# Kernel optimization log

Hardware: AMD Instinct MI355X
Metric: run time of the kernel (lower is better)

## Reference

```python
import jax, jax.numpy as jnp
import numpy as np

D_DIM = 1024
K_DIM = 16
B, L = 4, 2048

def setup_inputs() -> dict:
    key = jax.random.key(0)
    kx, ky, kz, kw, kb = jax.random.split(key, 5)
    x = jax.random.normal(kx, (B, L, D_DIM), dtype=jnp.float32)
    y = jax.random.normal(ky, (B, L, D_DIM), dtype=jnp.float32)
    z = jax.random.normal(kz, (B, L, D_DIM), dtype=jnp.float32)
    bound = 1.0 / np.sqrt(3 * D_DIM)  # torch Linear init scale
    W = jax.random.uniform(kw, (K_DIM * D_DIM, 3 * D_DIM), dtype=jnp.float32, minval=-bound, maxval=bound)
    b = jax.random.uniform(kb, (K_DIM * D_DIM,), dtype=jnp.float32, minval=-bound, maxval=bound)
    return {"x": x, "y": y, "z": z, "W": W, "b": b}

def reference(x, y, z, W, b):
    Bsz, Lsz, D = x.shape
    inp = jnp.concatenate([x, y, z], axis=-1)                 # (B, L, 3D)
    kernel = jnp.einsum('blc,fc->blf', inp, W) + b            # (B, L, k*D)
    kernel = kernel.reshape(Bsz, Lsz, D, K_DIM)               # (B, L, D, k)
    # einsum 'bldk,bld->bld' == sum over k, then elementwise multiply
    return kernel.sum(axis=-1) * (x * y)
```

## Files before the change

### kernel.cpp

```cpp
#include <hip/hip_runtime.h>

#define M_ROWS 8192
#define N_DIM  1024
#define K3     3072
#define KD     16
#define NKT    48
#define BM     256
#define BN     128
#define BK     64
#define LDS_A  (BM * BK)
#define LDS_B  (BN * BK)
#define LDS_TILE (LDS_A + LDS_B)

typedef __bf16 bf16x8 __attribute__((ext_vector_type(8)));
typedef float  f32x4  __attribute__((ext_vector_type(4)));

__device__ __forceinline__ unsigned short f2bf(float f) {
  return __builtin_bit_cast(unsigned short, (__bf16)f);
}
__device__ __forceinline__ float bf2f(unsigned short u) {
  return __builtin_bit_cast(float, (unsigned int)u << 16);
}
__device__ __forceinline__ ushort4 pack4(float4 f) {
  ushort4 o; o.x = f2bf(f.x); o.y = f2bf(f.y); o.z = f2bf(f.z); o.w = f2bf(f.w);
  return o;
}

__device__ __forceinline__ void async16(const void* g, void* l) {
  __builtin_amdgcn_global_load_lds(
      (const __attribute__((address_space(1))) unsigned int*)g,
      (__attribute__((address_space(3))) unsigned int*)l, 16, 0, 0);
}

__global__ __launch_bounds__(256) void wsum_kernel(
    const float* __restrict__ W, const float* __restrict__ b,
    ushort4* __restrict__ Wsum4, float* __restrict__ bsum)
{
  int bid = blockIdx.x;
  int tid = threadIdx.x;
  if (bid < 3072) {
    int g  = bid * 256 + tid;
    int d  = g / 768;
    int cq = g - d * 768;
    const float4* wrow = (const float4*)(W + (size_t)d * (KD * K3));
    float sx = 0.f, sy = 0.f, sz = 0.f, sw = 0.f;
    #pragma unroll
    for (int k = 0; k < KD; ++k) {
      float4 t = wrow[(size_t)k * (K3 / 4) + cq];
      sx += t.x; sy += t.y; sz += t.z; sw += t.w;
    }
    ushort4 o; o.x = f2bf(sx); o.y = f2bf(sy); o.z = f2bf(sz); o.w = f2bf(sw);
    Wsum4[g] = o;
  } else {
    int d = (bid - 3072) * 256 + tid;
    if (d < N_DIM) {
      float s = 0.f;
      #pragma unroll
      for (int k = 0; k < KD; ++k) s += b[d * KD + k];
      bsum[d] = s;
    }
  }
}

__global__ __launch_bounds__(256) void convert_kernel(
    const float4* __restrict__ x, const float4* __restrict__ y, const float4* __restrict__ z,
    ushort4* __restrict__ Ib4, ushort4* __restrict__ P4)
{
  int bid = blockIdx.x;
  int tid = threadIdx.x;
  int i = bid * 256 + tid;
  float4 fx = x[i], fy = y[i], fz = z[i];
  size_t rb = (size_t)bid * 768;
  Ib4[rb + tid]       = pack4(fx);
  Ib4[rb + 256 + tid] = pack4(fy);
  Ib4[rb + 512 + tid] = pack4(fz);
  float4 p; p.x = fx.x * fy.x; p.y = fx.y * fy.y; p.z = fx.z * fy.z; p.w = fx.w * fy.w;
  P4[i] = pack4(p);
}

__global__ __launch_bounds__(512, 2) void gemm_ep_kernel(
    const unsigned short* __restrict__ Ib, const unsigned short* __restrict__ Wsum,
    const float* __restrict__ bsum, const unsigned short* __restrict__ P,
    float* __restrict__ out)
{
  extern __shared__ unsigned short lds[];

  int bid = blockIdx.x;
  int swz = (bid & 7) * 32 + (bid >> 3);
  int mt = swz >> 3;
  int nt = swz & 7;
  int m0 = mt * BM, n0 = nt * BN;

  int tid  = threadIdx.x;
  int lane = tid & 63;
  int wid  = tid >> 6;
  int wr = wid >> 1, wc = wid & 1;

  int row0 = tid >> 3;
  int ch0  = tid & 7;
  int dofs = tid * 16;
  int sc   = ((ch0 ^ (row0 & 7)) << 3);

  const unsigned short* Abase = Ib   + (size_t)m0 * K3;
  const unsigned short* Bbase = Wsum + (size_t)n0 * K3;

  f32x4 acc[4][4];
  #pragma unroll
  for (int i = 0; i < 4; ++i)
    #pragma unroll
    for (int j = 0; j < 4; ++j)
      acc[i][j] = f32x4{0.f, 0.f, 0.f, 0.f};

  int fr = lane & 15;
  int hi = lane >> 4;

  auto STAGE_A = [&](int s, int t, int rlo, int rhi) {
    char* dst = (char*)(lds + s * LDS_TILE);
    int k0 = t << 6;
    for (int r = rlo; r < rhi; ++r)
      async16(Abase + (size_t)(row0 + r * 64) * K3 + k0 + sc, dst + dofs + r * 8192);
  };
  auto STAGE_B = [&](int s, int t, int rlo, int rhi) {
    char* dst = (char*)(lds + s * LDS_TILE) + 2 * LDS_A;
    int k0 = t << 6;
    for (int r = rlo; r < rhi; ++r)
      async16(Bbase + (size_t)(row0 + r * 64) * K3 + k0 + sc, dst + dofs + r * 8192);
  };

  bf16x8 a[4], b[4];
  auto LOADAB = [&](const unsigned short* pA, const unsigned short* pB, int kk) {
    int c = (kk << 2) + hi;
    #pragma unroll
    for (int i = 0; i < 4; ++i) {
      int R = wr * 64 + i * 16 + fr;
      a[i] = *(const bf16x8*)&pA[(R << 6) + ((c ^ (R & 7)) << 3)];
    }
    #pragma unroll
    for (int j = 0; j < 4; ++j) {
      int R = wc * 64 + j * 16 + fr;
      b[j] = *(const bf16x8*)&pB[(R << 6) + ((c ^ (R & 7)) << 3)];
    }
  };
  auto MFMA16 = [&]() {
    __builtin_amdgcn_s_setprio(1);
    #pragma unroll
    for (int i = 0; i < 4; ++i)
      #pragma unroll
      for (int j = 0; j < 4; ++j)
        acc[i][j] = __builtin_amdgcn_mfma_f32_16x16x32_bf16(a[i], b[j], acc[i][j], 0, 0, 0);
    __builtin_amdgcn_s_setprio(0);
  };

  STAGE_A(0, 0, 0, 4); STAGE_B(0, 0, 0, 2);
  STAGE_A(1, 1, 0, 4); STAGE_B(1, 1, 0, 2);
  asm volatile("s_waitcnt vmcnt(6)" ::: "memory");
  __builtin_amdgcn_s_barrier();

  for (int t = 0; t < NKT; ++t) {
    const unsigned short* pA = lds + (t % 3) * LDS_TILE;
    const unsigned short* pB = pA + LDS_A;
    int s2 = (t + 2) % 3;
    bool st = (t + 2) < NKT;

    LOADAB(pA, pB, 0);
    if (st) STAGE_A(s2, t + 2, 0, 3);
    __builtin_amdgcn_s_barrier();
    asm volatile("s_waitcnt lgkmcnt(0)" ::: "memory");
    __builtin_amdgcn_sched_barrier(0);
    MFMA16();
    __builtin_amdgcn_s_barrier();

    LOADAB(pA, pB, 1);
    if (st) { STAGE_A(s2, t + 2, 3, 4); STAGE_B(s2, t + 2, 0, 2); }
    if (st) asm volatile("s_waitcnt vmcnt(6)" ::: "memory");
    else    asm volatile("s_waitcnt vmcnt(0)" ::: "memory");
    __builtin_amdgcn_s_barrier();
    asm volatile("s_waitcnt lgkmcnt(0)" ::: "memory");
    __builtin_amdgcn_sched_barrier(0);
    MFMA16();
    __builtin_amdgcn_s_barrier();
  }

  #pragma unroll
  for (int i = 0; i < 4; ++i) {
    #pragma unroll
    for (int j = 0; j < 4; ++j) {
      int n = n0 + wc * 64 + j * 16 + fr;
      float bs = bsum[n];
      #pragma unroll
      for (int r = 0; r < 4; ++r) {
        int m = m0 + wr * 64 + i * 16 + hi * 4 + r;
        size_t idx = (size_t)m * N_DIM + n;
        out[idx] = (acc[i][j][r] + bs) * bf2f(P[idx]);
      }
    }
  }
}

extern "C" void kernel_launch(void* const* d_in, const int* in_sizes, int n_in,
                              void* d_out, int out_size, void* d_ws, size_t ws_size,
                              hipStream_t stream) {
  const float* x = (const float*)d_in[0];
  const float* y = (const float*)d_in[1];
  const float* z = (const float*)d_in[2];
  const float* W = (const float*)d_in[3];
  const float* b = (const float*)d_in[4];
  float* out = (float*)d_out;

  unsigned short* Ib   = (unsigned short*)d_ws;
  unsigned short* Wsum = Ib + (size_t)M_ROWS * K3;
  unsigned short* P    = Wsum + (size_t)N_DIM * K3;
  float*          bsum = (float*)(P + (size_t)M_ROWS * N_DIM);

  wsum_kernel<<<3076, 256, 0, stream>>>(W, b, (ushort4*)Wsum, bsum);

  convert_kernel<<<8192, 256, 0, stream>>>(
      (const float4*)x, (const float4*)y, (const float4*)z,
      (ushort4*)Ib, (ushort4*)P);

  gemm_ep_kernel<<<256, 512, 3 * LDS_TILE * sizeof(unsigned short), stream>>>(
      Ib, Wsum, bsum, P, out);
}
```

Before: 125.8 us.

## Double-buffer MFMA register fragments and unroll the K loop by three LDS slots

The main GEMM loop now keeps two sets of bf16 fragment registers. LDS reads for the next half-tile (or the next tile) are issued before the MFMAs on the current fragments run, and partial lgkmcnt waits are used in place of full drains. The loop is unrolled over the three LDS slots, which removes the modulo slot arithmetic and halves the number of barriers per K tile. All A and B staging for a tile is merged into one call. The cost is more VGPR pressure from the extra fragment buffers and tighter ordering assumptions around the waitcnt and barrier placement.

```diff
diff --git a/kernel.cpp b/kernel.cpp
--- a/kernel.cpp
+++ b/kernel.cpp
@@ -95,11 +95,13 @@
   int lane = tid & 63;
   int wid  = tid >> 6;
   int wr = wid >> 1, wc = wid & 1;
+  int fr = lane & 15;
+  int hi = lane >> 4;
 
   int row0 = tid >> 3;
   int ch0  = tid & 7;
   int dofs = tid * 16;
-  int sc   = ((ch0 ^ (row0 & 7)) << 3);
+  int sc   = (ch0 ^ (row0 & 7)) << 3;
 
   const unsigned short* Abase = Ib   + (size_t)m0 * K3;
   const unsigned short* Bbase = Wsum + (size_t)n0 * K3;
@@ -111,24 +113,20 @@
     for (int j = 0; j < 4; ++j)
       acc[i][j] = f32x4{0.f, 0.f, 0.f, 0.f};
 
-  int fr = lane & 15;
-  int hi = lane >> 4;
-
-  auto STAGE_A = [&](int s, int t, int rlo, int rhi) {
-    char* dst = (char*)(lds + s * LDS_TILE);
+  auto STAGE = [&](int slot, int t) {
+    char* dst = (char*)(lds + slot * LDS_TILE);
     int k0 = t << 6;
-    for (int r = rlo; r < rhi; ++r)
+    #pragma unroll
+    for (int r = 0; r < 4; ++r)
       async16(Abase + (size_t)(row0 + r * 64) * K3 + k0 + sc, dst + dofs + r * 8192);
-  };
-  auto STAGE_B = [&](int s, int t, int rlo, int rhi) {
-    char* dst = (char*)(lds + s * LDS_TILE) + 2 * LDS_A;
-    int k0 = t << 6;
-    for (int r = rlo; r < rhi; ++r)
-      async16(Bbase + (size_t)(row0 + r * 64) * K3 + k0 + sc, dst + dofs + r * 8192);
-  };
-
-  bf16x8 a[4], b[4];
-  auto LOADAB = [&](const unsigned short* pA, const unsigned short* pB, int kk) {
+    char* dstB = dst + 2 * LDS_A;
+    #pragma unroll
+    for (int r = 0; r < 2; ++r)
+      async16(Bbase + (size_t)(row0 + r * 64) * K3 + k0 + sc, dstB + dofs + r * 8192);
+  };
+
+  auto LOAD8 = [&](const unsigned short* pA, int kk, bf16x8 (&a)[4], bf16x8 (&b)[4]) {
+    const unsigned short* pB = pA + LDS_A;
     int c = (kk << 2) + hi;
     #pragma unroll
     for (int i = 0; i < 4; ++i) {
@@ -141,7 +139,7 @@
       b[j] = *(const bf16x8*)&pB[(R << 6) + ((c ^ (R & 7)) << 3)];
     }
   };
-  auto MFMA16 = [&]() {
+  auto MFMA16 = [&](bf16x8 (&a)[4], bf16x8 (&b)[4]) {
     __builtin_amdgcn_s_setprio(1);
     #pragma unroll
     for (int i = 0; i < 4; ++i)
@@ -151,34 +149,47 @@
     __builtin_amdgcn_s_setprio(0);
   };
 
-  STAGE_A(0, 0, 0, 4); STAGE_B(0, 0, 0, 2);
-  STAGE_A(1, 1, 0, 4); STAGE_B(1, 1, 0, 2);
+  bf16x8 aA[4], bA[4], aB[4], bB[4];
+
+  auto TILE = [&](int t, const unsigned short* pCur, const unsigned short* pNext,
+                  int stSlot) {
+    bool st = (t + 2) < NKT;
+    LOAD8(pCur, 1, aB, bB);
+    __builtin_amdgcn_sched_barrier(0);
+    if (st) {
+      STAGE(stSlot, t + 2);
+      asm volatile("s_waitcnt vmcnt(6)" ::: "memory");
+    } else {
+      asm volatile("s_waitcnt vmcnt(0)" ::: "memory");
+    }
+    asm volatile("s_waitcnt lgkmcnt(8)" ::: "memory");
+    __builtin_amdgcn_sched_barrier(0);
+    MFMA16(aA, bA);
+    __builtin_amdgcn_s_barrier();
+    LOAD8(pNext, 0, aA, bA);
+    __builtin_amdgcn_sched_barrier(0);
+    asm volatile("s_waitcnt lgkmcnt(8)" ::: "memory");
+    __builtin_amdgcn_sched_barrier(0);
+    MFMA16(aB, bB);
+    __builtin_amdgcn_s_barrier();
+  };
+
+  const unsigned short* s0 = lds;
+  const unsigned short* s1 = lds + LDS_TILE;
+  const unsigned short* s2 = lds + 2 * LDS_TILE;
+
+  STAGE(0, 0);
+  STAGE(1, 1);
   asm volatile("s_waitcnt vmcnt(6)" ::: "memory");
   __builtin_amdgcn_s_barrier();
-
-  for (int t = 0; t < NKT; ++t) {
-    const unsigned short* pA = lds + (t % 3) * LDS_TILE;
-    const unsigned short* pB = pA + LDS_A;
-    int s2 = (t + 2) % 3;
-    bool st = (t + 2) < NKT;
-
-    LOADAB(pA, pB, 0);
-    if (st) STAGE_A(s2, t + 2, 0, 3);
-    __builtin_amdgcn_s_barrier();
-    asm volatile("s_waitcnt lgkmcnt(0)" ::: "memory");
-    __builtin_amdgcn_sched_barrier(0);
-    MFMA16();
-    __builtin_amdgcn_s_barrier();
-
-    LOADAB(pA, pB, 1);
-    if (st) { STAGE_A(s2, t + 2, 3, 4); STAGE_B(s2, t + 2, 0, 2); }
-    if (st) asm volatile("s_waitcnt vmcnt(6)" ::: "memory");
-    else    asm volatile("s_waitcnt vmcnt(0)" ::: "memory");
-    __builtin_amdgcn_s_barrier();
-    asm volatile("s_waitcnt lgkmcnt(0)" ::: "memory");
-    __builtin_amdgcn_sched_barrier(0);
-    MFMA16();
-    __builtin_amdgcn_s_barrier();
+  LOAD8(s0, 0, aA, bA);
+  __builtin_amdgcn_sched_barrier(0);
+
+  #pragma unroll 1
+  for (int t = 0; t < NKT; t += 3) {
+    TILE(t,     s0, s1, 2);
+    TILE(t + 1, s1, s2, 0);
+    TILE(t + 2, s2, s0, 1);
   }
 
   #pragma unroll
```

Result: faster. 121.9 us (-3.1%).
